# Kernel optimization log

Hardware: AMD Instinct MI355X
Metric: run time of the kernel (lower is better)

## Reference

```python
import jax, jax.numpy as jnp
import numpy as np

WIDTH = 16       # beam width (self.width); WIDTH <= V+1 so K == WIDTH at every step
NORMALIZE = True
V_SIZE = 8000
D_MODEL = 1024
T_STEPS = 24
N_BATCH = 16


def setup_inputs() -> dict:
    key = jax.random.key(0)
    k1, k2, k3 = jax.random.split(key, 3)
    return {
        "N": N_BATCH,
        "T": T_STEPS,
        "token_emb": jax.random.normal(k1, (V_SIZE + 1, D_MODEL), jnp.float32) * 0.02,
        "time_emb": jax.random.normal(k2, (T_STEPS, D_MODEL), jnp.float32) * 0.02,
        "out_proj": jax.random.normal(k3, (D_MODEL, V_SIZE + 1), jnp.float32) * 0.02,
    }


def _lm_logits(token_emb, time_emb, out_proj, y_flat, t):
    # minimal stateless joint LM: condition on previous latent token + timestep
    V = token_emb.shape[0] - 1
    prev_tok = jnp.where(t > 0, y_flat[jnp.maximum(t - 1, 0)], V)  # (N*Kp,)
    h = token_emb[prev_tok] + time_emb[t]                           # (N*Kp, D)
    return h @ out_proj                                             # (N*Kp, V+1)


def _step(params, state, t):
    token_emb, time_emb, out_proj = params
    probs_prev, y_prev, y_prev_cond, y_prev_lens, prev_is_prefix = state
    T, N, Kp = y_prev.shape
    V = token_emb.shape[0] - 1
    K = WIDTH  # == min(width, Kp*(V+1)) because WIDTH <= V+1

    logits = _lm_logits(token_emb, time_emb, out_proj, y_prev.reshape(T, N * Kp), t)
    probs_t = jax.nn.softmax(logits.reshape(N, Kp, V + 1), axis=2)
    ext_probs = probs_t[..., :V] * probs_prev[:, :, None]  # (N,Kp,V)
    nonext = probs_t[..., V] * probs_prev                   # (N,Kp)

    nI = jnp.arange(N)[:, None, None]
    iI = jnp.arange(Kp)[None, :, None]
    jI = jnp.arange(Kp)[None, None, :]
    # tok_to_match[n,i,j] = token of hyp j at position len(i)
    tok_to_match = y_prev_cond[y_prev_lens[:, :, None], nI, jI]  # (N,Kp,Kp)
    ext_is_exact = ((y_prev_lens + 1)[:, :, None] == y_prev_lens[:, None, :]) & prev_is_prefix
    # has_match[n,i,v] = any_j(ext_is_exact[n,i,j] & tok_to_match[n,i,j]==v)
    has_match = jnp.zeros((N, Kp, V), jnp.int32).at[nI, iI, tok_to_match].add(
        ext_is_exact.astype(jnp.int32)) > 0
    gathered = jnp.take_along_axis(ext_probs, tok_to_match, axis=2)  # (N,Kp,Kp)
    nonext = nonext + jnp.sum(jnp.where(ext_is_exact, gathered, 0.0), axis=1)
    ext_probs = jnp.where(has_match, -jnp.inf, ext_probs)

    probs_cand = jnp.concatenate([ext_probs.reshape(N, Kp * V), nonext], axis=1)
    probs_next, next_idx = jax.lax.top_k(probs_cand, K)
    next_is_nonext = next_idx >= Kp * V
    next_src = jnp.where(next_is_nonext, next_idx - Kp * V, next_idx // V)
    next_ext = next_idx % V

    y_next_prefix_lens = jnp.take_along_axis(y_prev_lens, next_src, axis=1)  # (N,K)
    src3 = jnp.broadcast_to(next_src[None], (T, N, K))
    nK = jnp.arange(N)[:, None]
    kK = jnp.arange(K)[None, :]
    y_next_cond = jnp.take_along_axis(y_prev_cond, src3, axis=2)
    y_next_cond = y_next_cond.at[y_next_prefix_lens, nK, kK].set(next_ext)
    y_next = jnp.take_along_axis(y_prev, src3, axis=2)
    y_next = y_next.at[t].set(jnp.where(next_is_nonext, V, next_ext))
    y_next_lens = y_next_prefix_lens + (~next_is_nonext).astype(jnp.int32)

    nA = jnp.arange(N)[:, None, None]
    bI = jnp.arange(K)[None, None, :]
    next_prefix_is_prefix = prev_is_prefix[nA, next_src[:, :, None], next_src[:, None, :]]
    next_len_leq = y_next_lens[:, :, None] <= y_next_lens[:, None, :]
    next_to_match = y_next_cond[jnp.clip(y_next_lens - 1, 0)[:, :, None], nA, bI]
    next_ext_matches = next_to_match == next_ext[:, :, None]
    next_is_prefix = next_prefix_is_prefix & next_len_leq & (
        next_is_nonext[:, :, None] | (~next_is_nonext[:, :, None] & next_ext_matches))

    if NORMALIZE:
        probs_next = probs_next / jnp.max(probs_next, axis=1, keepdims=True)
    return (probs_next, y_next, y_next_cond, y_next_lens, next_is_prefix)


def _search(N, T, token_emb, time_emb, out_proj):
    V = token_emb.shape[0] - 1
    state = (jnp.ones((N, 1), jnp.float32),          # probs_prev
             jnp.full((T, N, 1), V, jnp.int32),      # y_prev (latent, V = blank)
             jnp.zeros((T, N, 1), jnp.int32),        # y_prev_cond
             jnp.zeros((N, 1), jnp.int32),           # y_prev_lens
             jnp.ones((N, 1, 1), bool))              # prev_is_prefix
    params = (token_emb, time_emb, out_proj)
    state = _step(params, state, jnp.int32(0))       # Kp: 1 -> WIDTH (static)

    def body(s, t):
        return _step(params, s, t), None

    state, _ = jax.lax.scan(body, state, jnp.arange(1, T))
    probs_prev, _, y_prev_cond, y_prev_lens, _ = state
    return y_prev_cond, y_prev_lens, probs_prev


def reference(N, T, token_emb, time_emb, out_proj):
    return _search(N, T, token_emb, time_emb, out_proj)
```

## Files before the change

### kernel.cpp

```cpp
#include <hip/hip_runtime.h>
#include <math.h>
#include <stdint.h>

#define NB 16
#define TT 24
#define VV 8000
#define VP1 8001
#define DD 1024
#define KW 16
#define MMAX 256
#define KSPLIT 4
#define KCHUNK 256

typedef unsigned long long u64;
typedef unsigned int u32;

__device__ __forceinline__ u64 packkey(float v, u32 idx) {
    return ((u64)__float_as_uint(v) << 32) | (u64)(0xFFFFFFFFu - idx);
}

__global__ __launch_bounds__(512, 2) void gemm_step(
    const float* __restrict__ tok_emb, const float* __restrict__ tim_emb,
    const float* __restrict__ W, const int* __restrict__ ylast,
    float* __restrict__ partial, int M, int t)
{
    __shared__ float As[2][16][256];
    __shared__ float Wt[2][16][64];
    const int tid = threadIdx.x;
    const int kc = blockIdx.y;
    const int kbase = kc * KCHUNK;

    int cbase = blockIdx.x * 64;
    if (cbase > VP1 - 64) cbase = VP1 - 64;
    const int tcol = tid & 15;
    const int trow = tid >> 4;
    const int c0 = cbase + tcol * 4;
    const int r0 = trow * 8;

    const int arow  = tid & 255;
    const int khalf = (tid >> 8) * 8;
    const int ptok = (t == 0) ? VV : ylast[arow];
    const float* __restrict__ ap = tok_emb + (size_t)ptok * DD + kbase + khalf;
    const float* __restrict__ tp = tim_emb + (size_t)t * DD + kbase + khalf;

    const int wk0 = tid >> 6;
    const int wc0 = tid & 63;
    const float* __restrict__ wp = W + (size_t)kbase * VP1 + cbase + wc0;

    float acc[8][4];
#pragma unroll
    for (int r = 0; r < 8; ++r)
#pragma unroll
        for (int c = 0; c < 4; ++c) acc[r][c] = 0.f;

    float4 a0 = *(const float4*)(ap);
    float4 a1 = *(const float4*)(ap + 4);
    float4 t0 = *(const float4*)(tp);
    float4 t1 = *(const float4*)(tp + 4);
    float w0 = wp[(size_t)wk0 * VP1];
    float w1 = wp[(size_t)(wk0 + 8) * VP1];

    for (int kt = 0; kt < KCHUNK; kt += 16) {
        const int buf = (kt >> 4) & 1;
        {
            float av[8] = { a0.x + t0.x, a0.y + t0.y, a0.z + t0.z, a0.w + t0.w,
                            a1.x + t1.x, a1.y + t1.y, a1.z + t1.z, a1.w + t1.w };
#pragma unroll
            for (int q = 0; q < 8; ++q) As[buf][khalf + q][arow] = av[q];
            Wt[buf][wk0][wc0]     = w0;
            Wt[buf][wk0 + 8][wc0] = w1;
        }
        __syncthreads();
        if (kt + 16 < KCHUNK) {
            a0 = *(const float4*)(ap + kt + 16);
            a1 = *(const float4*)(ap + kt + 20);
            t0 = *(const float4*)(tp + kt + 16);
            t1 = *(const float4*)(tp + kt + 20);
            w0 = wp[(size_t)(kt + 16 + wk0) * VP1];
            w1 = wp[(size_t)(kt + 16 + wk0 + 8) * VP1];
        }
#pragma unroll
        for (int k2 = 0; k2 < 16; ++k2) {
            const float4 wv = *(const float4*)(&Wt[buf][k2][tcol * 4]);
            float a8[8];
            *(float4*)(a8)     = *(const float4*)(&As[buf][k2][r0]);
            *(float4*)(a8 + 4) = *(const float4*)(&As[buf][k2][r0 + 4]);
#pragma unroll
            for (int r = 0; r < 8; ++r) {
                acc[r][0] = fmaf(a8[r], wv.x, acc[r][0]);
                acc[r][1] = fmaf(a8[r], wv.y, acc[r][1]);
                acc[r][2] = fmaf(a8[r], wv.z, acc[r][2]);
                acc[r][3] = fmaf(a8[r], wv.w, acc[r][3]);
            }
        }
    }

    float* __restrict__ outp = partial + (size_t)kc * ((size_t)MMAX * VP1);
#pragma unroll
    for (int r = 0; r < 8; ++r) {
        const int row = r0 + r;
        if (row < M) {
            float* __restrict__ op = outp + (size_t)row * VP1 + c0;
            op[0] = acc[r][0]; op[1] = acc[r][1];
            op[2] = acc[r][2]; op[3] = acc[r][3];
        }
    }
}

__global__ __launch_bounds__(256) void sm_topk1(
    const float* __restrict__ partial,
    const float* __restrict__ pprev, const int* __restrict__ mtok,
    float* __restrict__ scrv, int* __restrict__ scrc,
    float* __restrict__ rowmx, float* __restrict__ rowsc,
    int Kp)
{
    const int b = blockIdx.x;
    const int tid = threadIdx.x;
    const int lane = tid & 63, wid = tid >> 6;
    const int n = b / Kp, i = b % Kp;

    float l[32];
#pragma unroll
    for (int q = 0; q < 32; ++q) {
        int col = q * 256 + tid;
        float s = -INFINITY;
        if (col < VP1) {
            s = 0.f;
            for (int sp = 0; sp < KSPLIT; ++sp)
                s += partial[(size_t)sp * ((size_t)MMAX * VP1) + (size_t)b * VP1 + col];
        }
        l[q] = s;
    }
    float mx = -INFINITY;
#pragma unroll
    for (int q = 0; q < 32; ++q) mx = fmaxf(mx, l[q]);
#pragma unroll
    for (int off = 32; off; off >>= 1) mx = fmaxf(mx, __shfl_xor(mx, off));
    __shared__ float redf[4];
    if (lane == 0) redf[wid] = mx;
    __syncthreads();
    mx = fmaxf(fmaxf(redf[0], redf[1]), fmaxf(redf[2], redf[3]));
    float sum = 0.f;
#pragma unroll
    for (int q = 0; q < 32; ++q) {
        int col = q * 256 + tid;
        float e = (col < VP1) ? expf(l[q] - mx) : 0.f;
        l[q] = e; sum += e;
    }
#pragma unroll
    for (int off = 32; off; off >>= 1) sum += __shfl_xor(sum, off);
    __shared__ float reds[4];
    __syncthreads();
    if (lane == 0) reds[wid] = sum;
    __syncthreads();
    sum = reds[0] + reds[1] + reds[2] + reds[3];

    const float scale = pprev[n * KW + i] / sum;
    if (tid == 0) { rowmx[b] = mx; rowsc[b] = scale; }
#pragma unroll
    for (int q = 0; q < 32; ++q) {
        int col = q * 256 + tid;
        float p = l[q] * scale;
        l[q] = (col < VV) ? p : -1.0f;
    }

    {
        const int* __restrict__ mrow = mtok + (n * KW + i) * KW;
#pragma unroll
        for (int j = 0; j < KW; ++j) {
            int tk = mrow[j];
            if (tk >= 0 && (tk & 255) == tid) l[tk >> 8] = -1.0f;
        }
    }

    u32 taken = 0;
    float hv = -1.f; int hq = -1;
#pragma unroll
    for (int q = 0; q < 32; ++q)
        if (l[q] > hv) { hv = l[q]; hq = q; }

    __shared__ u64 wtop[4 * 16];
    for (int r = 0; r < 16; ++r) {
        u64 k = (hq < 0) ? 0ull : packkey(hv, (u32)(hq * 256 + tid));
        u64 m = k;
#pragma unroll
        for (int off = 32; off; off >>= 1) {
            u64 o = __shfl_xor(m, off);
            if (o > m) m = o;
        }
        if (lane == 0) wtop[wid * 16 + r] = m;
        if (m && k == m) {
            taken |= (1u << hq);
            hv = -1.f; hq = -1;
#pragma unroll
            for (int q = 0; q < 32; ++q)
                if (!((taken >> q) & 1u) && l[q] > hv) { hv = l[q]; hq = q; }
        }
    }
    __syncthreads();

    if (tid < 64) {
        u64 key = wtop[tid];
        for (int r = 0; r < 16; ++r) {
            u64 m = key;
#pragma unroll
            for (int off = 32; off; off >>= 1) {
                u64 o = __shfl_xor(m, off);
                if (o > m) m = o;
            }
            if (tid == 0) {
                scrv[b * 16 + r] = __uint_as_float((u32)(m >> 32));
                scrc[b * 16 + r] = (int)(0xFFFFFFFFu - (u32)m);
            }
            if (m && key == m) key = 0ull;
        }
    }
}

__device__ __forceinline__ float cand_at(const float* __restrict__ partial,
                                         int b, int col, float mx, float sc) {
    float s = 0.f;
#pragma unroll
    for (int sp = 0; sp < KSPLIT; ++sp)
        s += partial[(size_t)sp * ((size_t)MMAX * VP1) + (size_t)b * VP1 + col];
    return expf(s - mx) * sc;
}

__global__ __launch_bounds__(256) void topk2_update(
    const float* __restrict__ partial,
    const float* __restrict__ rowmx, const float* __restrict__ rowsc,
    const float* __restrict__ scrv, const int* __restrict__ scrc,
    const int* __restrict__ lens_in, const int* __restrict__ cond_in,
    const unsigned char* __restrict__ pref_in,
    float* __restrict__ pprev_out, int* __restrict__ lens_out,
    int* __restrict__ cond_out, unsigned char* __restrict__ pref_out,
    int* __restrict__ ylast, int* __restrict__ mtok, int Kp)
{
    const int n = blockIdx.x, tid = threadIdx.x;
    const int lane = tid & 63, wid = tid >> 6;
    const int i = tid >> 4, j = tid & 15;

    __shared__ int   s_lens[KW];
    __shared__ float s_rmx[KW], s_rsc[KW];
    __shared__ float s_g[KW * KW];
    __shared__ float s_nx[KW];

    if (tid < KW) s_lens[tid] = (tid < Kp) ? lens_in[n * KW + tid] : 0;
    if (tid < Kp) { s_rmx[tid] = rowmx[n * Kp + tid]; s_rsc[tid] = rowsc[n * Kp + tid]; }
    __syncthreads();

    {
        int tok = mtok[(n * KW + i) * KW + j];
        s_g[i * KW + j] = (tok >= 0)
            ? cand_at(partial, n * Kp + i, tok, s_rmx[i], s_rsc[i]) : 0.f;
    }
    __syncthreads();
    if (tid < Kp) {
        float s = cand_at(partial, n * Kp + tid, VV, s_rmx[tid], s_rsc[tid]);
        for (int ii = 0; ii < Kp; ++ii) s += s_g[ii * KW + tid];
        s_nx[tid] = s;
    }
    __syncthreads();

#define POOLN 272
    __shared__ u64 pool[POOLN];
    for (int e = tid; e < POOLN; e += 256) {
        u64 key = 0ull;
        if (e < Kp * 16) {
            int r = e >> 4, q = e & 15;
            float v = scrv[(n * Kp + r) * 16 + q];
            int col = scrc[(n * Kp + r) * 16 + q];
            key = packkey(v, (u32)(r * VV + col));
        } else if (e >= KW * 16 && e < KW * 16 + Kp) {
            int jj = e - KW * 16;
            key = packkey(s_nx[jj], (u32)(Kp * VV + jj));
        }
        pool[e] = key;
    }
    __syncthreads();

    __shared__ u64 s_top[KW];
    __shared__ u64 redk[4];
    for (int r = 0; r < KW; ++r) {
        u64 k0 = pool[tid];
        u64 k1 = (tid < 16) ? pool[tid + 256] : 0ull;
        u64 m = (k0 > k1) ? k0 : k1;
#pragma unroll
        for (int off = 32; off; off >>= 1) {
            u64 o = __shfl_xor(m, off);
            if (o > m) m = o;
        }
        if (lane == 0) redk[wid] = m;
        __syncthreads();
        m = redk[0];
        if (redk[1] > m) m = redk[1];
        if (redk[2] > m) m = redk[2];
        if (redk[3] > m) m = redk[3];
        if (tid == 0) s_top[r] = m;
        if (m) {
            if (pool[tid] == m)       pool[tid] = 0;
            if (tid < 16 && pool[tid + 256] == m) pool[tid + 256] = 0;
        }
        __syncthreads();
    }

    __shared__ int   s_src[KW], s_ext[KW], s_plen[KW], s_lnew[KW], s_nxt[KW];
    __shared__ float s_val[KW];
    if (tid < KW) {
        u64 m = s_top[tid];
        float v = __uint_as_float((u32)(m >> 32));
        int flat = (int)(0xFFFFFFFFu - (u32)m);
        int nx  = (flat >= Kp * VV) ? 1 : 0;
        int src = nx ? (flat - Kp * VV) : (flat / VV);
        int ext = flat % VV;
        s_src[tid] = src; s_ext[tid] = ext; s_nxt[tid] = nx; s_val[tid] = v;
        int pl = s_lens[src];
        s_plen[tid] = pl;
        int ln = pl + (nx ? 0 : 1);
        s_lnew[tid] = ln;
        lens_out[n * KW + tid] = ln;
        ylast[n * KW + tid] = nx ? VV : ext;
    }
    __syncthreads();
    if (tid < KW) pprev_out[n * KW + tid] = s_val[tid] / s_val[0];

    __shared__ int s_cond[TT * KW];
    for (int x = tid; x < TT * KW; x += 256) {
        int k = x & 15;
        s_cond[x] = cond_in[(x >> 4) * (NB * KW) + n * KW + s_src[k]];
    }
    __syncthreads();
    if (tid < KW) s_cond[s_plen[tid] * KW + tid] = s_ext[tid];
    __syncthreads();
    for (int x = tid; x < TT * KW; x += 256)
        cond_out[(x >> 4) * (NB * KW) + n * KW + (x & 15)] = s_cond[x];

    {
        bool p = (pref_in[(n * KW + s_src[i]) * KW + s_src[j]] != 0)
              && (s_lnew[i] <= s_lnew[j]);
        if (p && !s_nxt[i]) {
            int pos = s_lnew[i] - 1; if (pos < 0) pos = 0;
            p = (s_cond[pos * KW + j] == s_ext[i]);
        }
        pref_out[(n * KW + i) * KW + j] = p ? 1 : 0;

        int li = s_lnew[i];
        bool exn = p && (li + 1 == s_lnew[j]);
        int pos2 = (li < TT) ? li : (TT - 1);
        mtok[(n * KW + i) * KW + j] = exn ? s_cond[pos2 * KW + j] : -1;
    }
}

__global__ __launch_bounds__(256) void init_state(
    float* pprev0, int* lens0, int* cond0, unsigned char* pref0, int* mtok)
{
    int idx = blockIdx.x * 256 + threadIdx.x;
    if (idx < TT * NB * KW) cond0[idx] = 0;
    if (idx < NB * KW) { lens0[idx] = 0; pprev0[idx] = 1.0f; }
    if (idx < NB * KW * KW) { pref0[idx] = 1; mtok[idx] = -1; }
}

__global__ __launch_bounds__(256) void finalize_out(
    const int* __restrict__ cond0, const int* __restrict__ lens0,
    const float* __restrict__ pprev0, float* __restrict__ out)
{
    int idx = blockIdx.x * 256 + threadIdx.x;
    const int A = TT * NB * KW, B = NB * KW;
    if (idx < A) out[idx] = (float)cond0[idx];
    else if (idx < A + B) out[idx] = (float)lens0[idx - A];
    else if (idx < A + 2 * B) out[idx] = pprev0[idx - A - B];
}

extern "C" void kernel_launch(void* const* d_in, const int* in_sizes, int n_in,
                              void* d_out, int out_size, void* d_ws, size_t ws_size,
                              hipStream_t stream)
{
    const float* tok = (const float*)d_in[2];
    const float* tim = (const float*)d_in[3];
    const float* W   = (const float*)d_in[4];

    char* ws = (char*)d_ws;
    size_t off = 0;
    auto alloc = [&](size_t bytes) -> void* {
        void* p = ws + off;
        off = (off + bytes + 255) & ~(size_t)255;
        return p;
    };
    const size_t partBytes = (size_t)MMAX * VP1 * sizeof(float);

    float* partial = (float*)alloc((size_t)KSPLIT * partBytes);
    float* scrv    = (float*)alloc((size_t)MMAX * 16 * sizeof(float));
    int*   scrc    = (int*)  alloc((size_t)MMAX * 16 * sizeof(int));
    float* rowmx   = (float*)alloc((size_t)MMAX * sizeof(float));
    float* rowsc   = (float*)alloc((size_t)MMAX * sizeof(float));
    float* pprev[2]; int* lens[2]; int* cond[2]; unsigned char* pref[2];
    for (int p = 0; p < 2; ++p) {
        pprev[p] = (float*)alloc(NB * KW * sizeof(float));
        lens[p]  = (int*)  alloc(NB * KW * sizeof(int));
        cond[p]  = (int*)  alloc((size_t)TT * NB * KW * sizeof(int));
        pref[p]  = (unsigned char*)alloc(NB * KW * KW);
    }
    int* ylast = (int*)alloc(NB * KW * sizeof(int));
    int* mtok  = (int*)alloc((size_t)NB * KW * KW * sizeof(int));

    init_state<<<(TT * NB * KW + 255) / 256, 256, 0, stream>>>(
        pprev[0], lens[0], cond[0], pref[0], mtok);

    for (int t = 0; t < TT; ++t) {
        const int Kp = t ? KW : 1;
        const int M  = NB * Kp;
        const int in = t & 1, out = in ^ 1;
        gemm_step<<<dim3(126, KSPLIT), 512, 0, stream>>>(
            tok, tim, W, ylast, partial, M, t);
        sm_topk1<<<M, 256, 0, stream>>>(
            partial, pprev[in], mtok, scrv, scrc, rowmx, rowsc, Kp);
        topk2_update<<<NB, 256, 0, stream>>>(
            partial, rowmx, rowsc, scrv, scrc, lens[in], cond[in], pref[in],
            pprev[out], lens[out], cond[out], pref[out], ylast, mtok, Kp);
    }
    finalize_out<<<(TT * NB * KW + 2 * NB * KW + 255) / 256, 256, 0, stream>>>(
        cond[0], lens[0], pprev[0], (float*)d_out);
}
```

Before: 2.467 ms.

## Split GEMM rows into 128-row blocks and skip inactive row blocks

The per-step GEMM now uses 256-thread blocks covering 128 rows, with the grid's y dimension encoding both the K-split chunk and the row block. Row blocks beyond M return early and threads whose rows exceed M skip the FMA loop, so the t=0 step (M=16) does far less wasted compute. For full steps this doubles the block count and lowers per-block shared memory, which raises occupancy. The cost is that each W tile is now loaded twice, once per row block.

```diff
diff --git a/kernel.cpp b/kernel.cpp
--- a/kernel.cpp
+++ b/kernel.cpp
@@ -19,15 +19,17 @@
     return ((u64)__float_as_uint(v) << 32) | (u64)(0xFFFFFFFFu - idx);
 }
 
-__global__ __launch_bounds__(512, 2) void gemm_step(
+__global__ __launch_bounds__(256, 4) void gemm_step(
     const float* __restrict__ tok_emb, const float* __restrict__ tim_emb,
     const float* __restrict__ W, const int* __restrict__ ylast,
     float* __restrict__ partial, int M, int t)
 {
-    __shared__ float As[2][16][256];
+    __shared__ float As[2][16][128];
     __shared__ float Wt[2][16][64];
     const int tid = threadIdx.x;
-    const int kc = blockIdx.y;
+    const int kc = blockIdx.y & 3;
+    const int rb = blockIdx.y >> 2;
+    if (rb * 128 >= M) return;
     const int kbase = kc * KCHUNK;
 
     int cbase = blockIdx.x * 64;
@@ -35,15 +37,18 @@
     const int tcol = tid & 15;
     const int trow = tid >> 4;
     const int c0 = cbase + tcol * 4;
-    const int r0 = trow * 8;
-
-    const int arow  = tid & 255;
-    const int khalf = (tid >> 8) * 8;
-    const int ptok = (t == 0) ? VV : ylast[arow];
+    const int lr0 = trow * 8;
+    const int r0 = rb * 128 + lr0;
+    const bool active = (r0 < M);
+
+    const int arow  = tid & 127;
+    const int khalf = (tid >> 7) * 8;
+    const int grow = rb * 128 + arow;
+    const int ptok = (t == 0) ? VV : ylast[grow];
     const float* __restrict__ ap = tok_emb + (size_t)ptok * DD + kbase + khalf;
     const float* __restrict__ tp = tim_emb + (size_t)t * DD + kbase + khalf;
 
-    const int wk0 = tid >> 6;
+    const int wr  = tid >> 6;
     const int wc0 = tid & 63;
     const float* __restrict__ wp = W + (size_t)kbase * VP1 + cbase + wc0;
 
@@ -57,8 +62,10 @@
     float4 a1 = *(const float4*)(ap + 4);
     float4 t0 = *(const float4*)(tp);
     float4 t1 = *(const float4*)(tp + 4);
-    float w0 = wp[(size_t)wk0 * VP1];
-    float w1 = wp[(size_t)(wk0 + 8) * VP1];
+    float w0 = wp[(size_t)(wr) * VP1];
+    float w1 = wp[(size_t)(wr + 4) * VP1];
+    float w2 = wp[(size_t)(wr + 8) * VP1];
+    float w3 = wp[(size_t)(wr + 12) * VP1];
 
     for (int kt = 0; kt < KCHUNK; kt += 16) {
         const int buf = (kt >> 4) & 1;
@@ -67,8 +74,10 @@
                             a1.x + t1.x, a1.y + t1.y, a1.z + t1.z, a1.w + t1.w };
 #pragma unroll
             for (int q = 0; q < 8; ++q) As[buf][khalf + q][arow] = av[q];
-            Wt[buf][wk0][wc0]     = w0;
-            Wt[buf][wk0 + 8][wc0] = w1;
+            Wt[buf][wr][wc0]      = w0;
+            Wt[buf][wr + 4][wc0]  = w1;
+            Wt[buf][wr + 8][wc0]  = w2;
+            Wt[buf][wr + 12][wc0] = w3;
         }
         __syncthreads();
         if (kt + 16 < KCHUNK) {
@@ -76,21 +85,25 @@
             a1 = *(const float4*)(ap + kt + 20);
             t0 = *(const float4*)(tp + kt + 16);
             t1 = *(const float4*)(tp + kt + 20);
-            w0 = wp[(size_t)(kt + 16 + wk0) * VP1];
-            w1 = wp[(size_t)(kt + 16 + wk0 + 8) * VP1];
-        }
-#pragma unroll
-        for (int k2 = 0; k2 < 16; ++k2) {
-            const float4 wv = *(const float4*)(&Wt[buf][k2][tcol * 4]);
-            float a8[8];
-            *(float4*)(a8)     = *(const float4*)(&As[buf][k2][r0]);
-            *(float4*)(a8 + 4) = *(const float4*)(&As[buf][k2][r0 + 4]);
-#pragma unroll
-            for (int r = 0; r < 8; ++r) {
-                acc[r][0] = fmaf(a8[r], wv.x, acc[r][0]);
-                acc[r][1] = fmaf(a8[r], wv.y, acc[r][1]);
-                acc[r][2] = fmaf(a8[r], wv.z, acc[r][2]);
-                acc[r][3] = fmaf(a8[r], wv.w, acc[r][3]);
+            w0 = wp[(size_t)(kt + 16 + wr) * VP1];
+            w1 = wp[(size_t)(kt + 16 + wr + 4) * VP1];
+            w2 = wp[(size_t)(kt + 16 + wr + 8) * VP1];
+            w3 = wp[(size_t)(kt + 16 + wr + 12) * VP1];
+        }
+        if (active) {
+#pragma unroll
+            for (int k2 = 0; k2 < 16; ++k2) {
+                const float4 wv = *(const float4*)(&Wt[buf][k2][tcol * 4]);
+                float a8[8];
+                *(float4*)(a8)     = *(const float4*)(&As[buf][k2][lr0]);
+                *(float4*)(a8 + 4) = *(const float4*)(&As[buf][k2][lr0 + 4]);
+#pragma unroll
+                for (int r = 0; r < 8; ++r) {
+                    acc[r][0] = fmaf(a8[r], wv.x, acc[r][0]);
+                    acc[r][1] = fmaf(a8[r], wv.y, acc[r][1]);
+                    acc[r][2] = fmaf(a8[r], wv.z, acc[r][2]);
+                    acc[r][3] = fmaf(a8[r], wv.w, acc[r][3]);
+                }
             }
         }
     }
@@ -410,7 +423,7 @@
         const int Kp = t ? KW : 1;
         const int M  = NB * Kp;
         const int in = t & 1, out = in ^ 1;
-        gemm_step<<<dim3(126, KSPLIT), 512, 0, stream>>>(
+        gemm_step<<<dim3(126, 8), 256, 0, stream>>>(
             tok, tim, W, ylast, partial, M, t);
         sm_topk1<<<M, 256, 0, stream>>>(
             partial, pprev[in], mtok, scrv, scrc, rowmx, rowsc, Kp);
```

Result: slower. 2.537 ms (+2.9%).
